# Kernel tuning notes

Hardware: AMD Instinct MI355X
Metric: run time of the kernel (lower is better)

The kernel has to match this reference:

```python
import jax, jax.numpy as jnp
import numpy as np

B, T, D = 2048, 200, 64
H1, H2 = 80, 40
NEG_INF = -4294967295.0  # -(2**32) + 1 as in original


def setup_inputs() -> dict:
    key0 = jax.random.key(0)
    ks = jax.random.split(key0, 10)
    din_dim = 4 * D
    inp = {
        "query": jax.random.normal(ks[0], (B, D), dtype=jnp.float32),
        "key": jax.random.normal(ks[1], (B, T, D), dtype=jnp.float32),
        "mask": jax.random.randint(ks[2], (B,), 1, T + 1, dtype=jnp.int32),
        # MLP params (Dense 4D->80->40->1, use_bias=True)
        "W1": jax.random.normal(ks[3], (din_dim, H1), dtype=jnp.float32) / np.sqrt(din_dim),
        "b1": jnp.zeros((H1,), dtype=jnp.float32),
        "W2": jax.random.normal(ks[4], (H1, H2), dtype=jnp.float32) / np.sqrt(H1),
        "b2": jnp.zeros((H2,), dtype=jnp.float32),
        "W3": jax.random.normal(ks[5], (H2, 1), dtype=jnp.float32) / np.sqrt(H2),
        "b3": jnp.zeros((1,), dtype=jnp.float32),
    }
    return inp


def reference(query, key, mask, W1, b1, W2, b2, W3, b3):
    b, t, d = key.shape
    q = query[:, None, :]                      # [B,1,D]
    q_tile = jnp.broadcast_to(q, (b, t, d))    # [B,T,D]
    din_all = jnp.concatenate([q_tile, key, q_tile - key, q_tile * key], axis=-1)  # [B,T,4D]
    h = jax.nn.sigmoid(jnp.einsum("btf,fh->bth", din_all, W1) + b1)
    h = jax.nn.sigmoid(jnp.einsum("bth,hg->btg", h, W2) + b2)
    score = (jnp.einsum("btg,go->bto", h, W3) + b3)[..., 0]  # [B,T]
    key_mask = jnp.arange(t)[None, :] < mask[:, None]        # [B,T]
    score = jnp.where(key_mask, score, NEG_INF)
    score = score / jnp.asarray(d, score.dtype) ** 0.5
    attn = jax.nn.softmax(score, axis=-1)                    # [B,T]
    out = jnp.einsum("bt,btd->bd", attn, key)                # [B,D] (squeezed)
    return out
```

## Files before the change

### kernel.cpp

```cpp
#include <hip/hip_runtime.h>
#include <math.h>

#define B_  2048
#define T_  200
#define D_  64
#define H1_ 80
#define H2_ 40

#define VSTR 72
#define WSTR 104
#define HSTR 104

#define WS_A    0
#define WS_C    10240
#define WS_W2T  20480
#define WS_ACT  30464

typedef __bf16 bf16x8 __attribute__((ext_vector_type(8)));
typedef float  f32x4  __attribute__((ext_vector_type(4)));

__device__ __forceinline__ float sigmoidf_(float x) {
    return __builtin_amdgcn_rcpf(1.0f + __expf(-x));
}

__global__ __launch_bounds__(256)
void prep_kernel(const float* __restrict__ W1, const float* __restrict__ W2,
                 void* __restrict__ ws)
{
    __bf16* A    = (__bf16*)((char*)ws + WS_A);
    __bf16* C    = (__bf16*)((char*)ws + WS_C);
    __bf16* W2Tp = (__bf16*)((char*)ws + WS_W2T);
    float*  acT  = (float*)((char*)ws + WS_ACT);
    const int e0 = blockIdx.x * 256 + threadIdx.x;

    for (int e = e0; e < H1_ * D_; e += 2048) {
        int h = e >> 6, f = e & 63;
        float wb = W1[(64  + f) * H1_ + h];
        float wc = W1[(128 + f) * H1_ + h];
        float wd = W1[(192 + f) * H1_ + h];
        float wa = W1[f * H1_ + h];
        A[e]   = (__bf16)(wb - wc);
        C[e]   = (__bf16)wd;
        acT[e] = wa + wc;
    }
    for (int e = e0; e < 48 * WSTR; e += 2048) {
        int g = e / WSTR, h = e - g * WSTR;
        W2Tp[e] = (g < H2_ && h < H1_) ? (__bf16)W2[h * H2_ + g] : (__bf16)0.0f;
    }
}

__global__ __launch_bounds__(128, 3)
void attn_din12(const float* __restrict__ query,
                const float* __restrict__ key,
                const int*   __restrict__ mask,
                const float* __restrict__ b1,
                const float* __restrict__ b2,
                const float* __restrict__ W3,
                const float* __restrict__ b3,
                const void*  __restrict__ ws,
                float* __restrict__ out)
{
    __shared__ __align__(16) __bf16 s_V[H1_ * VSTR];
    __shared__ __align__(16) __bf16 s_h1[2][16 * HSTR];
    __shared__ float s_scf[208];
    __shared__ float s_q[D_];
    __shared__ float s_base[H1_];
    __shared__ float s_part[2][D_];
    __shared__ float s_red[4];

    const int tid  = threadIdx.x;
    const int lane = tid & 63;
    const int w    = tid >> 6;
    const int c16  = lane & 15;
    const int g16  = lane >> 4;
    const int b    = blockIdx.x;

    const int   mv     = mask[b];
    const int   ntiles = (mv + 15) >> 4;
    const float b3v    = b3[0];
    const float* kb = key + (size_t)b * T_ * D_;

    const __bf16* wsA   = (const __bf16*)((const char*)ws + WS_A);
    const __bf16* wsC   = (const __bf16*)((const char*)ws + WS_C);
    const __bf16* wsW2T = (const __bf16*)((const char*)ws + WS_W2T);
    const float*  wsacT = (const float*) ((const char*)ws + WS_ACT);

    if (w == 0) s_q[lane] = query[b * D_ + lane];
    for (int i = tid; i < 208; i += 128) s_scf[i] = -1e30f;

    bf16x8 bw[3][3];
    #pragma unroll
    for (int nt = 0; nt < 3; ++nt)
        #pragma unroll
        for (int ks = 0; ks < 3; ++ks)
            bw[nt][ks] = *(const bf16x8*)&wsW2T[(nt * 16 + c16) * WSTR + ks * 32 + g16 * 8];

    float b2c[3], w3c[3];
    #pragma unroll
    for (int nt = 0; nt < 3; ++nt) {
        int g = nt * 16 + c16;
        b2c[nt] = (g < H2_) ? b2[g] : 0.0f;
        w3c[nt] = (g < H2_) ? W3[g] : 0.0f;
    }
    __syncthreads();

    #pragma unroll
    for (int i = 0; i < 5; ++i) {
        int e = tid + 128 * i;
        int h = e >> 3, f8 = e & 7;
        bf16x8 a8 = *(const bf16x8*)&wsA[e * 8];
        bf16x8 c8 = *(const bf16x8*)&wsC[e * 8];
        f32x4 q0 = *(const f32x4*)&s_q[f8 * 8];
        f32x4 q1 = *(const f32x4*)&s_q[f8 * 8 + 4];
        bf16x8 v8;
        v8[0] = (__bf16)((float)a8[0] + q0[0] * (float)c8[0]);
        v8[1] = (__bf16)((float)a8[1] + q0[1] * (float)c8[1]);
        v8[2] = (__bf16)((float)a8[2] + q0[2] * (float)c8[2]);
        v8[3] = (__bf16)((float)a8[3] + q0[3] * (float)c8[3]);
        v8[4] = (__bf16)((float)a8[4] + q1[0] * (float)c8[4]);
        v8[5] = (__bf16)((float)a8[5] + q1[1] * (float)c8[5]);
        v8[6] = (__bf16)((float)a8[6] + q1[2] * (float)c8[6]);
        v8[7] = (__bf16)((float)a8[7] + q1[3] * (float)c8[7]);
        *(bf16x8*)&s_V[h * VSTR + f8 * 8] = v8;
    }

    if (tid < H1_) {
        float a0 = b1[tid], a1 = 0.0f, a2 = 0.0f, a3 = 0.0f;
        const f32x4* row = (const f32x4*)&wsacT[tid * D_];
        #pragma unroll
        for (int f4 = 0; f4 < 16; ++f4) {
            f32x4 v  = row[f4];
            f32x4 q4 = *(const f32x4*)&s_q[f4 * 4];
            a0 = fmaf(q4[0], v[0], a0);
            a1 = fmaf(q4[1], v[1], a1);
            a2 = fmaf(q4[2], v[2], a2);
            a3 = fmaf(q4[3], v[3], a3);
        }
        s_base[tid] = (a0 + a1) + (a2 + a3);
    }

    {
        int row = lane & 15, c0 = 80 + (lane >> 4) * 4;
        *(uint2*)&s_h1[w][row * HSTR + c0] = make_uint2(0u, 0u);
    }
    __syncthreads();

    float base_c[5];
    #pragma unroll
    for (int nt = 0; nt < 5; ++nt) base_c[nt] = s_base[nt * 16 + c16];
    __bf16* myh = &s_h1[w][0];

    float4 u0, u1, u2, u3;
    {
        int tr = w * 16 + c16;
        const float* kr = kb + (size_t)((tr < T_) ? tr : (T_ - 1)) * D_ + g16 * 8;
        u0 = *(const float4*)(kr);
        u1 = *(const float4*)(kr + 4);
        u2 = *(const float4*)(kr + 32);
        u3 = *(const float4*)(kr + 36);
    }

    for (int tt = w; tt < ntiles; tt += 2) {
        bf16x8 af0, af1;
        af0[0] = (__bf16)u0.x; af0[1] = (__bf16)u0.y; af0[2] = (__bf16)u0.z; af0[3] = (__bf16)u0.w;
        af0[4] = (__bf16)u1.x; af0[5] = (__bf16)u1.y; af0[6] = (__bf16)u1.z; af0[7] = (__bf16)u1.w;
        af1[0] = (__bf16)u2.x; af1[1] = (__bf16)u2.y; af1[2] = (__bf16)u2.z; af1[3] = (__bf16)u2.w;
        af1[4] = (__bf16)u3.x; af1[5] = (__bf16)u3.y; af1[6] = (__bf16)u3.z; af1[7] = (__bf16)u3.w;

        if (tt + 2 < ntiles) {
            int tr = (tt + 2) * 16 + c16;
            const float* kr = kb + (size_t)((tr < T_) ? tr : (T_ - 1)) * D_ + g16 * 8;
            u0 = *(const float4*)(kr);
            u1 = *(const float4*)(kr + 4);
            u2 = *(const float4*)(kr + 32);
            u3 = *(const float4*)(kr + 36);
        }

        #pragma unroll
        for (int nt = 0; nt < 5; ++nt) {
            float bb = base_c[nt];
            f32x4 c = { bb, bb, bb, bb };
            bf16x8 bv0 = *(const bf16x8*)&s_V[(nt * 16 + c16) * VSTR + g16 * 8];
            bf16x8 bv1 = *(const bf16x8*)&s_V[(nt * 16 + c16) * VSTR + 32 + g16 * 8];
            c = __builtin_amdgcn_mfma_f32_16x16x32_bf16(af0, bv0, c, 0, 0, 0);
            c = __builtin_amdgcn_mfma_f32_16x16x32_bf16(af1, bv1, c, 0, 0, 0);
            #pragma unroll
            for (int r = 0; r < 4; ++r)
                myh[(g16 * 4 + r) * HSTR + nt * 16 + c16] = (__bf16)sigmoidf_(c[r]);
        }

        bf16x8 a2_0 = *(const bf16x8*)&myh[c16 * HSTR + g16 * 8];
        bf16x8 a2_1 = *(const bf16x8*)&myh[c16 * HSTR + 32 + g16 * 8];
        bf16x8 a2_2 = *(const bf16x8*)&myh[c16 * HSTR + 64 + g16 * 8];
        f32x4 acc2[3];
        #pragma unroll
        for (int nt = 0; nt < 3; ++nt) {
            float bb = b2c[nt];
            f32x4 c = { bb, bb, bb, bb };
            c = __builtin_amdgcn_mfma_f32_16x16x32_bf16(a2_0, bw[nt][0], c, 0, 0, 0);
            c = __builtin_amdgcn_mfma_f32_16x16x32_bf16(a2_1, bw[nt][1], c, 0, 0, 0);
            c = __builtin_amdgcn_mfma_f32_16x16x32_bf16(a2_2, bw[nt][2], c, 0, 0, 0);
            acc2[nt] = c;
        }

        const int tb = tt * 16;
        #pragma unroll
        for (int r = 0; r < 4; ++r) {
            float partial = sigmoidf_(acc2[0][r]) * w3c[0]
                          + sigmoidf_(acc2[1][r]) * w3c[1]
                          + sigmoidf_(acc2[2][r]) * w3c[2];
            partial += __shfl_xor(partial, 1);
            partial += __shfl_xor(partial, 2);
            partial += __shfl_xor(partial, 4);
            partial += __shfl_xor(partial, 8);
            int t = tb + g16 * 4 + r;
            if (c16 == 0 && t < mv)
                s_scf[t] = (partial + b3v) * 0.125f;
        }
    }
    __syncthreads();

    float s0 = s_scf[tid];
    float s1 = (tid + 128 < 208) ? s_scf[tid + 128] : -1e30f;
    float m = fmaxf(s0, s1);
    #pragma unroll
    for (int off = 32; off >= 1; off >>= 1) m = fmaxf(m, __shfl_xor(m, off));
    if (lane == 0) s_red[w] = m;
    __syncthreads();
    m = fmaxf(s_red[0], s_red[1]);
    float p0 = __expf(s0 - m);
    float p1 = (tid + 128 < 208) ? __expf(s1 - m) : 0.0f;
    float ps = p0 + p1;
    #pragma unroll
    for (int off = 32; off >= 1; off >>= 1) ps += __shfl_xor(ps, off);
    if (lane == 0) s_red[2 + w] = ps;
    __syncthreads();
    float inv_total = __builtin_amdgcn_rcpf(s_red[2] + s_red[3]);
    s_scf[tid] = p0;
    if (tid + 128 < 208) s_scf[tid + 128] = p1;
    __syncthreads();

    float a0 = 0.0f, a1 = 0.0f, a2s = 0.0f, a3s = 0.0f;
    for (int tt = w; tt < ntiles; tt += 2) {
        int t0 = tt * 16;
        int tend = (t0 + 16 < mv) ? (t0 + 16) : mv;
        int t = t0;
        for (; t + 4 <= tend; t += 4) {
            a0  = fmaf(s_scf[t],     kb[(t)     * D_ + lane], a0);
            a1  = fmaf(s_scf[t + 1], kb[(t + 1) * D_ + lane], a1);
            a2s = fmaf(s_scf[t + 2], kb[(t + 2) * D_ + lane], a2s);
            a3s = fmaf(s_scf[t + 3], kb[(t + 3) * D_ + lane], a3s);
        }
        for (; t < tend; ++t)
            a0 = fmaf(s_scf[t], kb[t * D_ + lane], a0);
    }
    s_part[w][lane] = (a0 + a1) + (a2s + a3s);
    __syncthreads();
    if (tid < D_)
        out[b * D_ + tid] = (s_part[0][tid] + s_part[1][tid]) * inv_total;
}

extern "C" void kernel_launch(void* const* d_in, const int* in_sizes, int n_in,
                              void* d_out, int out_size, void* d_ws, size_t ws_size,
                              hipStream_t stream)
{
    const float* query = (const float*)d_in[0];
    const float* key   = (const float*)d_in[1];
    const int*   mask  = (const int*)  d_in[2];
    const float* W1    = (const float*)d_in[3];
    const float* b1    = (const float*)d_in[4];
    const float* W2    = (const float*)d_in[5];
    const float* b2    = (const float*)d_in[6];
    const float* W3    = (const float*)d_in[7];
    const float* b3    = (const float*)d_in[8];
    float* out = (float*)d_out;

    prep_kernel<<<8, 256, 0, stream>>>(W1, W2, d_ws);
    attn_din12<<<B_, 128, 0, stream>>>(query, key, mask, b1, b2, W3, b3, d_ws, out);
}
```

Baseline: 51.63 us.

## Fuse online softmax and weighted key sum into the MLP tile loop

Computes softmax with a running max and running sum for each 16-row tile, inside the same loop that computes the scores. The weighted sum over keys reuses the key values already held in registers, so key no longer has to be read from global memory a second time. This also drops the score buffer and several block-wide barriers and reductions. The cost is extra exponentials and cross-lane shuffles per tile, and the output sum now uses bf16-rounded key values instead of the fp32 inputs, which lowers accuracy.

```diff
diff --git a/kernel.cpp b/kernel.cpp
--- a/kernel.cpp
+++ b/kernel.cpp
@@ -50,7 +50,7 @@
 }
 
 __global__ __launch_bounds__(128, 3)
-void attn_din12(const float* __restrict__ query,
+void attn_din13(const float* __restrict__ query,
                 const float* __restrict__ key,
                 const int*   __restrict__ mask,
                 const float* __restrict__ b1,
@@ -62,11 +62,11 @@
 {
     __shared__ __align__(16) __bf16 s_V[H1_ * VSTR];
     __shared__ __align__(16) __bf16 s_h1[2][16 * HSTR];
-    __shared__ float s_scf[208];
-    __shared__ float s_q[D_];
+    __shared__ __align__(16) float  s_q[D_];
     __shared__ float s_base[H1_];
+    __shared__ float s_sc16[2][16];
     __shared__ float s_part[2][D_];
-    __shared__ float s_red[4];
+    __shared__ float s_ml[2][2];
 
     const int tid  = threadIdx.x;
     const int lane = tid & 63;
@@ -85,8 +85,7 @@
     const __bf16* wsW2T = (const __bf16*)((const char*)ws + WS_W2T);
     const float*  wsacT = (const float*) ((const char*)ws + WS_ACT);
 
-    if (w == 0) s_q[lane] = query[b * D_ + lane];
-    for (int i = tid; i < 208; i += 128) s_scf[i] = -1e30f;
+    if (tid < D_) s_q[tid] = query[b * D_ + tid];
 
     bf16x8 bw[3][3];
     #pragma unroll
@@ -160,6 +159,10 @@
         u3 = *(const float4*)(kr + 36);
     }
 
+    float o00,o01,o02,o03,o04,o05,o06,o07,o08,o09,o10,o11,o12,o13,o14,o15;
+    o00=o01=o02=o03=o04=o05=o06=o07=o08=o09=o10=o11=o12=o13=o14=o15=0.0f;
+    float m_run = -1e30f, l_run = 0.0f;
+
     for (int tt = w; tt < ntiles; tt += 2) {
         bf16x8 af0, af1;
         af0[0] = (__bf16)u0.x; af0[1] = (__bf16)u0.y; af0[2] = (__bf16)u0.z; af0[3] = (__bf16)u0.w;
@@ -213,51 +216,66 @@
             partial += __shfl_xor(partial, 2);
             partial += __shfl_xor(partial, 4);
             partial += __shfl_xor(partial, 8);
-            int t = tb + g16 * 4 + r;
-            if (c16 == 0 && t < mv)
-                s_scf[t] = (partial + b3v) * 0.125f;
-        }
-    }
+            if (c16 == 0) {
+                int t = tb + g16 * 4 + r;
+                s_sc16[w][g16 * 4 + r] = (t < mv) ? (partial + b3v) * 0.125f : -1e30f;
+            }
+        }
+
+        float s = s_sc16[w][c16];
+        float tm = s;
+        tm = fmaxf(tm, __shfl_xor(tm, 1));
+        tm = fmaxf(tm, __shfl_xor(tm, 2));
+        tm = fmaxf(tm, __shfl_xor(tm, 4));
+        tm = fmaxf(tm, __shfl_xor(tm, 8));
+        float m_new = fmaxf(m_run, tm);
+        float alpha = __expf(m_run - m_new);
+        float p = __expf(s - m_new);
+        float psum = p;
+        psum += __shfl_xor(psum, 1);
+        psum += __shfl_xor(psum, 2);
+        psum += __shfl_xor(psum, 4);
+        psum += __shfl_xor(psum, 8);
+        l_run = l_run * alpha + psum;
+        o00 = fmaf(p, (float)af0[0], o00 * alpha);  o01 = fmaf(p, (float)af0[1], o01 * alpha);
+        o02 = fmaf(p, (float)af0[2], o02 * alpha);  o03 = fmaf(p, (float)af0[3], o03 * alpha);
+        o04 = fmaf(p, (float)af0[4], o04 * alpha);  o05 = fmaf(p, (float)af0[5], o05 * alpha);
+        o06 = fmaf(p, (float)af0[6], o06 * alpha);  o07 = fmaf(p, (float)af0[7], o07 * alpha);
+        o08 = fmaf(p, (float)af1[0], o08 * alpha);  o09 = fmaf(p, (float)af1[1], o09 * alpha);
+        o10 = fmaf(p, (float)af1[2], o10 * alpha);  o11 = fmaf(p, (float)af1[3], o11 * alpha);
+        o12 = fmaf(p, (float)af1[4], o12 * alpha);  o13 = fmaf(p, (float)af1[5], o13 * alpha);
+        o14 = fmaf(p, (float)af1[6], o14 * alpha);  o15 = fmaf(p, (float)af1[7], o15 * alpha);
+        m_run = m_new;
+    }
+
+    #define ORED(X) X += __shfl_xor(X,1); X += __shfl_xor(X,2); X += __shfl_xor(X,4); X += __shfl_xor(X,8);
+    ORED(o00) ORED(o01) ORED(o02) ORED(o03) ORED(o04) ORED(o05) ORED(o06) ORED(o07)
+    ORED(o08) ORED(o09) ORED(o10) ORED(o11) ORED(o12) ORED(o13) ORED(o14) ORED(o15)
+    #undef ORED
+    if (c16 == 0) {
+        float* sp = &s_part[w][0];
+        sp[g16 * 8 + 0] = o00;  sp[g16 * 8 + 1] = o01;
+        sp[g16 * 8 + 2] = o02;  sp[g16 * 8 + 3] = o03;
+        sp[g16 * 8 + 4] = o04;  sp[g16 * 8 + 5] = o05;
+        sp[g16 * 8 + 6] = o06;  sp[g16 * 8 + 7] = o07;
+        sp[32 + g16 * 8 + 0] = o08;  sp[32 + g16 * 8 + 1] = o09;
+        sp[32 + g16 * 8 + 2] = o10;  sp[32 + g16 * 8 + 3] = o11;
+        sp[32 + g16 * 8 + 4] = o12;  sp[32 + g16 * 8 + 5] = o13;
+        sp[32 + g16 * 8 + 6] = o14;  sp[32 + g16 * 8 + 7] = o15;
+    }
+    if (lane == 0) { s_ml[w][0] = m_run; s_ml[w][1] = l_run; }
     __syncthreads();
 
-    float s0 = s_scf[tid];
-    float s1 = (tid + 128 < 208) ? s_scf[tid + 128] : -1e30f;
-    float m = fmaxf(s0, s1);
-    #pragma unroll
-    for (int off = 32; off >= 1; off >>= 1) m = fmaxf(m, __shfl_xor(m, off));
-    if (lane == 0) s_red[w] = m;
-    __syncthreads();
-    m = fmaxf(s_red[0], s_red[1]);
-    float p0 = __expf(s0 - m);
-    float p1 = (tid + 128 < 208) ? __expf(s1 - m) : 0.0f;
-    float ps = p0 + p1;
-    #pragma unroll
-    for (int off = 32; off >= 1; off >>= 1) ps += __shfl_xor(ps, off);
-    if (lane == 0) s_red[2 + w] = ps;
-    __syncthreads();
-    float inv_total = __builtin_amdgcn_rcpf(s_red[2] + s_red[3]);
-    s_scf[tid] = p0;
-    if (tid + 128 < 208) s_scf[tid + 128] = p1;
-    __syncthreads();
-
-    float a0 = 0.0f, a1 = 0.0f, a2s = 0.0f, a3s = 0.0f;
-    for (int tt = w; tt < ntiles; tt += 2) {
-        int t0 = tt * 16;
-        int tend = (t0 + 16 < mv) ? (t0 + 16) : mv;
-        int t = t0;
-        for (; t + 4 <= tend; t += 4) {
-            a0  = fmaf(s_scf[t],     kb[(t)     * D_ + lane], a0);
-            a1  = fmaf(s_scf[t + 1], kb[(t + 1) * D_ + lane], a1);
-            a2s = fmaf(s_scf[t + 2], kb[(t + 2) * D_ + lane], a2s);
-            a3s = fmaf(s_scf[t + 3], kb[(t + 3) * D_ + lane], a3s);
-        }
-        for (; t < tend; ++t)
-            a0 = fmaf(s_scf[t], kb[t * D_ + lane], a0);
-    }
-    s_part[w][lane] = (a0 + a1) + (a2s + a3s);
-    __syncthreads();
-    if (tid < D_)
-        out[b * D_ + tid] = (s_part[0][tid] + s_part[1][tid]) * inv_total;
+    if (tid < D_) {
+        float m0 = s_ml[0][0], l0 = s_ml[0][1];
+        float m1 = s_ml[1][0], l1 = s_ml[1][1];
+        float mm = fmaxf(m0, m1);
+        float f0 = __expf(m0 - mm);
+        float f1 = __expf(m1 - mm);
+        float tot = l0 * f0 + l1 * f1;
+        out[b * D_ + tid] = (s_part[0][tid] * f0 + s_part[1][tid] * f1)
+                          * __builtin_amdgcn_rcpf(tot);
+    }
 }
 
 extern "C" void kernel_launch(void* const* d_in, const int* in_sizes, int n_in,
@@ -276,5 +294,5 @@
     float* out = (float*)d_out;
 
     prep_kernel<<<8, 256, 0, stream>>>(W1, W2, d_ws);
-    attn_din12<<<B_, 128, 0, stream>>>(query, key, mask, b1, b2, W3, b3, d_ws, out);
-}
+    attn_din13<<<B_, 128, 0, stream>>>(query, key, mask, b1, b2, W3, b3, d_ws, out);
+}
```

Result: slower. 62.98 us (+22.0%).
